# Kernel tuning notes

Measured on AMD Instinct MI355X. Metric: run time of the kernel, lower is better.

Reference implementation:

```python
import jax, jax.numpy as jnp
import numpy as np

NUM_CATS = 5
EPS = 1e-6


def setup_inputs() -> dict:
    key = jax.random.key(0)
    k1, k2, k3, k4 = jax.random.split(key, 4)
    B, C, H, W = 64, 3, 256, 256
    restored = jax.random.normal(k1, (B, C, H, W), dtype=jnp.float32)
    clean_patch_1 = jax.random.normal(k2, (B, C, H, W), dtype=jnp.float32)
    un = jax.random.uniform(k3, (B, C, H, W), dtype=jnp.float32)
    de_id = jax.random.randint(k4, (B,), 0, NUM_CATS)
    return {"restored": restored, "clean_patch_1": clean_patch_1,
            "de_id": de_id, "un": un}


def _loss(restored, clean, un, de_id):
    B, C, H, W = restored.shape
    E = C * H * W  # elements per sample
    dt = restored.dtype

    onehot = (de_id[:, None] == jnp.arange(NUM_CATS)[None, :])  # [B,5] bool
    m = onehot.astype(dt)                                        # [B,5]
    counts = onehot.sum(0)                                       # [5] int
    nonempty = counts > 0
    safe_counts = jnp.maximum(counts, 1).astype(dt)              # avoid 0-div

    # Per-category mean uncertainty map: un_map[c] = mean_{i: de_id[i]=c} un[i] + eps
    un_sum = jnp.einsum('bk,bchw->kchw', m, un)                  # [5,C,H,W]
    un_map = un_sum / safe_counts[:, None, None, None] + EPS     # [5,C,H,W]
    s = 1.0 / un_map                                             # [5,C,H,W]

    # Per-sample scaled L1 (s gathered by each sample's category)
    absdiff = jnp.abs(clean - restored)                          # [B,C,H,W]
    scaled_sum_per_sample = (absdiff * s[de_id]).sum(axis=(1, 2, 3))  # [B]
    abs_sum_per_sample = absdiff.sum(axis=(1, 2, 3))                  # [B]

    cat_scaled_sum = jnp.einsum('bk,b->k', m, scaled_sum_per_sample)  # [5]
    cat_abs_sum = jnp.einsum('bk,b->k', m, abs_sum_per_sample)        # [5]

    # NOTE: the original code never clears un_hq_list/un_lq_list between
    # categories, so the L1 at category c is the mean over ALL samples from
    # categories 0..c (each scaled by its OWN category's s). Replicate that
    # via cumulative sums/counts over the category axis.
    cum_scaled = jnp.cumsum(cat_scaled_sum)                      # [5]
    cum_elems = jnp.cumsum(counts).astype(dt) * E                # [5]
    cum_l1 = cum_scaled / jnp.maximum(cum_elems, 1.0)            # [5]

    old_loss = jnp.where(nonempty, cat_abs_sum / (safe_counts * E), 0.0)
    un_num = un_map.mean(axis=(1, 2, 3))                         # [5]
    bn = jnp.where(nonempty, 2.0 * jnp.log(un_num), 0.0)
    unc_l1 = jnp.where(nonempty, cum_l1, 0.0)

    cat_losses = unc_l1 + bn                                     # [5]
    num = nonempty.sum().astype(dt)
    total = cat_losses.sum() / num
    return total, cat_losses, old_loss, bn, unc_l1


def reference(restored, clean_patch_1, de_id, un):
    return _loss(restored, clean_patch_1, un, de_id)
```

## Files before the change

### kernel.cpp

```cpp
#include <hip/hip_runtime.h>
#include <math.h>

#define NCAT  5
#define BATCH 64
#define ELEMS 196608
#define EPSV  1e-6f

typedef float v4f __attribute__((ext_vector_type(4)));

#define WIN   1024
#define WIN4  (WIN / 4)
#define NCHK  4
#define NBLK1 (ELEMS / WIN)
#define CHUNK 16
#define GRP   4

#define NSLAB  12
#define SLABSZ (ELEMS / NSLAB)
#define NBLK2  (BATCH * NSLAB)

#define WS_S   0
#define WS_P1  (NCAT * ELEMS)
#define WS_P2  (WS_P1 + NCAT * NBLK1)

static __device__ __forceinline__ v4f vfma(float m, v4f a, v4f b) {
    v4f r;
    r.x = fmaf(m, a.x, b.x);
    r.y = fmaf(m, a.y, b.y);
    r.z = fmaf(m, a.z, b.z);
    r.w = fmaf(m, a.w, b.w);
    return r;
}

__global__ __launch_bounds__(256, 1) void pass1_kernel(
    const float* __restrict__ un,
    const int*   __restrict__ de_id,
    float*       __restrict__ s_buf,
    float*       __restrict__ p1)
{
    __shared__ int   sh_de[BATCH];
    __shared__ float sh_inv[NCAT];
    __shared__ v4f   sbuf[2][NCAT][WIN4];

    const int tid  = threadIdx.x;
    const int lane = tid & 63;
    const int wave = tid >> 6;

    if (tid < BATCH) {
        int k = de_id[tid];
        sh_de[tid] = k;
        #pragma unroll
        for (int j = 0; j < NCAT; ++j) {
            unsigned long long m = __ballot(k == j);
            if (tid == j) {
                int c = __popcll(m);
                sh_inv[j] = 1.0f / (float)(c > 0 ? c : 1);
            }
        }
    }
    __syncthreads();

    const size_t STR4 = ELEMS / 4;
    const v4f* up4 = (const v4f*)(un) + (size_t)blockIdx.x * WIN4 + lane;

    v4f acc[NCAT][NCHK];
    #pragma unroll
    for (int j = 0; j < NCAT; ++j)
        #pragma unroll
        for (int c = 0; c < NCHK; ++c) acc[j][c] = (v4f)0.f;

    v4f ub[2][GRP][NCHK];
    #pragma unroll
    for (int i = 0; i < GRP; ++i)
        #pragma unroll
        for (int c = 0; c < NCHK; ++c)
            ub[0][i][c] = up4[(size_t)(wave * CHUNK + i) * STR4 + c * 64];

    #pragma unroll
    for (int g = 0; g < CHUNK / GRP; ++g) {
        const int cur = g & 1;
        const int nxt = cur ^ 1;
        if (g < CHUNK / GRP - 1) {
            #pragma unroll
            for (int i = 0; i < GRP; ++i)
                #pragma unroll
                for (int c = 0; c < NCHK; ++c)
                    ub[nxt][i][c] =
                        up4[(size_t)(wave * CHUNK + (g + 1) * GRP + i) * STR4 + c * 64];
        }
        #pragma unroll
        for (int i = 0; i < GRP; ++i) {
            const int k = sh_de[wave * CHUNK + g * GRP + i];
            #pragma unroll
            for (int j = 0; j < NCAT; ++j) {
                float m = (k == j) ? 1.0f : 0.0f;
                #pragma unroll
                for (int c = 0; c < NCHK; ++c)
                    acc[j][c] = vfma(m, ub[cur][i][c], acc[j][c]);
            }
        }
    }

    if (wave >= 2) {
        #pragma unroll
        for (int j = 0; j < NCAT; ++j)
            #pragma unroll
            for (int c = 0; c < NCHK; ++c)
                sbuf[wave - 2][j][c * 64 + lane] = acc[j][c];
    }
    __syncthreads();
    if (wave < 2) {
        #pragma unroll
        for (int j = 0; j < NCAT; ++j)
            #pragma unroll
            for (int c = 0; c < NCHK; ++c)
                acc[j][c] += sbuf[wave][j][c * 64 + lane];
    }
    __syncthreads();
    if (wave == 1) {
        #pragma unroll
        for (int j = 0; j < NCAT; ++j)
            #pragma unroll
            for (int c = 0; c < NCHK; ++c)
                sbuf[0][j][c * 64 + lane] = acc[j][c];
    }
    __syncthreads();
    if (wave == 0) {
        float vals[NCAT];
        #pragma unroll
        for (int j = 0; j < NCAT; ++j) {
            float tot = 0.f;
            #pragma unroll
            for (int c = 0; c < NCHK; ++c) {
                v4f a = acc[j][c] + sbuf[0][j][c * 64 + lane];

                v4f um;
                um.x = fmaf(a.x, sh_inv[j], EPSV);
                um.y = fmaf(a.y, sh_inv[j], EPSV);
                um.z = fmaf(a.z, sh_inv[j], EPSV);
                um.w = fmaf(a.w, sh_inv[j], EPSV);
                v4f sv;
                sv.x = 1.0f / um.x;
                sv.y = 1.0f / um.y;
                sv.z = 1.0f / um.z;
                sv.w = 1.0f / um.w;
                ((v4f*)s_buf)[(size_t)j * STR4 + (size_t)blockIdx.x * WIN4
                              + c * 64 + lane] = sv;

                tot += (a.x + a.y) + (a.z + a.w);
            }
            vals[j] = tot;
        }

        #pragma unroll
        for (int i = 0; i < NCAT; ++i) {
            float v = vals[i];
            #pragma unroll
            for (int off = 32; off >= 1; off >>= 1)
                v += __shfl_down(v, off, 64);
            vals[i] = v;
        }
        if (lane == 0) {
            #pragma unroll
            for (int i = 0; i < NCAT; ++i)
                p1[i * NBLK1 + blockIdx.x] = vals[i];
        }
    }
}

__global__ __launch_bounds__(256) void pass2_kernel(
    const float* __restrict__ restored,
    const float* __restrict__ clean,
    const int*   __restrict__ de_id,
    const float* __restrict__ s_buf,
    float*       __restrict__ p2)
{
    __shared__ float sred[4][2];

    const int tid  = threadIdx.x;
    const int lane = tid & 63;
    const int wave = tid >> 6;

    const int b   = blockIdx.x / NSLAB;
    const int sl  = blockIdx.x % NSLAB;
    const int cat = de_id[b];

    const size_t base4 = (size_t)sl * (SLABSZ / 4) + (size_t)wave * (SLABSZ / 16)
                       + (size_t)lane;
    const v4f* cp = (const v4f*)(clean)    + (size_t)b   * (ELEMS / 4) + base4;
    const v4f* rp = (const v4f*)(restored) + (size_t)b   * (ELEMS / 4) + base4;
    const v4f* sp = (const v4f*)(s_buf)    + (size_t)cat * (ELEMS / 4) + base4;

    float ssum = 0.f, asum = 0.f;
    #pragma unroll 16
    for (int it = 0; it < SLABSZ / 16 / 64; ++it) {
        v4f c  = __builtin_nontemporal_load(cp + it * 64);
        v4f r  = __builtin_nontemporal_load(rp + it * 64);
        v4f sv = sp[it * 64];
        float a0 = fabsf(c.x - r.x);
        float a1 = fabsf(c.y - r.y);
        float a2 = fabsf(c.z - r.z);
        float a3 = fabsf(c.w - r.w);
        asum += (a0 + a1) + (a2 + a3);
        ssum = fmaf(a0, sv.x, ssum);
        ssum = fmaf(a1, sv.y, ssum);
        ssum = fmaf(a2, sv.z, ssum);
        ssum = fmaf(a3, sv.w, ssum);
    }

    #pragma unroll
    for (int off = 32; off >= 1; off >>= 1) {
        ssum += __shfl_down(ssum, off, 64);
        asum += __shfl_down(asum, off, 64);
    }
    if (lane == 0) { sred[wave][0] = ssum; sred[wave][1] = asum; }
    __syncthreads();
    if (tid == 0) {
        float s = sred[0][0] + sred[1][0] + sred[2][0] + sred[3][0];
        float a = sred[0][1] + sred[1][1] + sred[2][1] + sred[3][1];
        p2[blockIdx.x]         = s;
        p2[NBLK2 + blockIdx.x] = a;
    }
}

__global__ __launch_bounds__(1024) void epilogue_kernel(
    const int*   __restrict__ de_id,
    const float* __restrict__ p1,
    const float* __restrict__ p2,
    float*       __restrict__ out)
{
    __shared__ int   sh_cnt[NCAT];
    __shared__ int   sh_cat[BATCH];
    __shared__ float sh_acc[3 * NCAT];

    const int tid  = threadIdx.x;
    const int lane = tid & 63;
    const int wave = tid >> 6;

    if (tid < BATCH) {
        int k = de_id[tid];
        sh_cat[tid] = k;
        #pragma unroll
        for (int j = 0; j < NCAT; ++j) {
            unsigned long long m = __ballot(k == j);
            if (tid == j) sh_cnt[j] = __popcll(m);
        }
    }
    __syncthreads();

    float v = 0.f;
    if (wave < 5) {
        for (int it = 0; it < NBLK2 / 64; ++it) {
            int col = it * 64 + lane;
            v += (sh_cat[col / NSLAB] == wave) ? p2[col] : 0.f;
        }
    } else if (wave < 10) {
        const int j = wave - 5;
        for (int it = 0; it < NBLK2 / 64; ++it) {
            int col = it * 64 + lane;
            v += (sh_cat[col / NSLAB] == j) ? p2[NBLK2 + col] : 0.f;
        }
    } else if (wave < 15) {
        const int j = wave - 10;
        for (int it = 0; it < NBLK1 / 64; ++it)
            v += p1[j * NBLK1 + it * 64 + lane];
    }
    #pragma unroll
    for (int off = 32; off >= 1; off >>= 1)
        v += __shfl_down(v, off, 64);
    if (lane == 0 && wave < 15) sh_acc[wave] = v;
    __syncthreads();

    if (tid == 0) {
        const float Ef = (float)ELEMS;
        float cum_s = 0.f;
        long  cum_c = 0;
        float total = 0.f;
        int   num   = 0;

        float cat_losses[NCAT], old_loss[NCAT], bn[NCAT], unc_l1[NCAT];

        for (int j = 0; j < NCAT; ++j) {
            cum_s += sh_acc[j];
            cum_c += sh_cnt[j];
            float cum_elems = (float)cum_c * Ef;
            float cum_l1    = cum_s / fmaxf(cum_elems, 1.0f);

            bool  ne   = sh_cnt[j] > 0;
            float safe = (float)(ne ? sh_cnt[j] : 1);

            old_loss[j]  = ne ? sh_acc[NCAT + j] / (safe * Ef) : 0.f;
            float un_num = sh_acc[2 * NCAT + j] / (safe * Ef) + EPSV;
            bn[j]        = ne ? 2.0f * logf(un_num) : 0.f;
            unc_l1[j]    = ne ? cum_l1 : 0.f;
            cat_losses[j] = unc_l1[j] + bn[j];
            total += cat_losses[j];
            num   += ne ? 1 : 0;
        }
        total /= (float)num;

        out[0] = total;
        for (int j = 0; j < NCAT; ++j) {
            out[1 + j]  = cat_losses[j];
            out[6 + j]  = old_loss[j];
            out[11 + j] = bn[j];
            out[16 + j] = unc_l1[j];
        }
    }
}

extern "C" void kernel_launch(void* const* d_in, const int* in_sizes, int n_in,
                              void* d_out, int out_size, void* d_ws, size_t ws_size,
                              hipStream_t stream) {
    (void)in_sizes; (void)n_in; (void)out_size; (void)ws_size;
    const float* restored = (const float*)d_in[0];
    const float* clean    = (const float*)d_in[1];
    const int*   de_id    = (const int*)d_in[2];
    const float* un       = (const float*)d_in[3];
    float* out   = (float*)d_out;
    float* ws    = (float*)d_ws;
    float* s_buf = ws + WS_S;
    float* p1    = ws + WS_P1;
    float* p2    = ws + WS_P2;

    pass1_kernel<<<NBLK1, 256, 0, stream>>>(un, de_id, s_buf, p1);
    pass2_kernel<<<NBLK2, 256, 0, stream>>>(restored, clean, de_id, s_buf, p2);
    epilogue_kernel<<<1, 1024, 0, stream>>>(de_id, p1, p2, out);
}
```

Measured before the change: 168.8 us.

## Widen pass1 to 1024 threads and fold epilogue into pass2 via last-block atomic

Pass1 now runs 1024 threads per block, with each wave covering 64 float4 columns instead of four chunks. This cuts per-thread register use and raises the number of waves in flight for the un reduction. The separate epilogue launch is removed: the last pass2 block, detected with an atomic counter reset in pass1, performs the final category reduction. This saves one kernel launch and its serial gap, but adds a threadfence and an atomic to every pass2 block.

```diff
diff --git a/kernel.cpp b/kernel.cpp
--- a/kernel.cpp
+++ b/kernel.cpp
@@ -8,12 +8,11 @@
 
 typedef float v4f __attribute__((ext_vector_type(4)));
 
-#define WIN   1024
-#define WIN4  (WIN / 4)
-#define NCHK  4
-#define NBLK1 (ELEMS / WIN)
-#define CHUNK 16
-#define GRP   4
+#define WIN1   1024
+#define NBLK1  (ELEMS / WIN1)
+#define TPB1   1024
+#define CHUNK1 16
+#define GRP1   8
 
 #define NSLAB  12
 #define SLABSZ (ELEMS / NSLAB)
@@ -22,6 +21,7 @@
 #define WS_S   0
 #define WS_P1  (NCAT * ELEMS)
 #define WS_P2  (WS_P1 + NCAT * NBLK1)
+#define WS_CNT (WS_P2 + 2 * NBLK2)
 
 static __device__ __forceinline__ v4f vfma(float m, v4f a, v4f b) {
     v4f r;
@@ -32,19 +32,25 @@
     return r;
 }
 
-__global__ __launch_bounds__(256, 1) void pass1_kernel(
+__global__ __launch_bounds__(TPB1) void pass1_kernel(
     const float* __restrict__ un,
     const int*   __restrict__ de_id,
     float*       __restrict__ s_buf,
-    float*       __restrict__ p1)
+    float*       __restrict__ p1,
+    unsigned*    __restrict__ cnt)
 {
     __shared__ int   sh_de[BATCH];
     __shared__ float sh_inv[NCAT];
-    __shared__ v4f   sbuf[2][NCAT][WIN4];
+    __shared__ v4f   sbuf[2][4][NCAT][64];
+    __shared__ float sh_part[4][NCAT];
 
     const int tid  = threadIdx.x;
     const int lane = tid & 63;
     const int wave = tid >> 6;
+    const int ws   = wave & 3;
+    const int bc   = wave >> 2;
+
+    if (blockIdx.x == 0 && tid == 0) *cnt = 0u;
 
     if (tid < BATCH) {
         int k = de_id[tid];
@@ -61,111 +67,85 @@
     __syncthreads();
 
     const size_t STR4 = ELEMS / 4;
-    const v4f* up4 = (const v4f*)(un) + (size_t)blockIdx.x * WIN4 + lane;
-
-    v4f acc[NCAT][NCHK];
+    const size_t pos4 = (size_t)blockIdx.x * (WIN1 / 4) + ws * 64 + lane;
+    const v4f* up4 = (const v4f*)(un) + pos4;
+
+    v4f acc[NCAT];
     #pragma unroll
-    for (int j = 0; j < NCAT; ++j)
-        #pragma unroll
-        for (int c = 0; c < NCHK; ++c) acc[j][c] = (v4f)0.f;
-
-    v4f ub[2][GRP][NCHK];
+    for (int j = 0; j < NCAT; ++j) acc[j] = (v4f)0.f;
+
+    v4f ub[2][GRP1];
     #pragma unroll
-    for (int i = 0; i < GRP; ++i)
-        #pragma unroll
-        for (int c = 0; c < NCHK; ++c)
-            ub[0][i][c] = up4[(size_t)(wave * CHUNK + i) * STR4 + c * 64];
+    for (int i = 0; i < GRP1; ++i)
+        ub[0][i] = up4[(size_t)(bc * CHUNK1 + i) * STR4];
 
     #pragma unroll
-    for (int g = 0; g < CHUNK / GRP; ++g) {
+    for (int g = 0; g < CHUNK1 / GRP1; ++g) {
         const int cur = g & 1;
         const int nxt = cur ^ 1;
-        if (g < CHUNK / GRP - 1) {
-            #pragma unroll
-            for (int i = 0; i < GRP; ++i)
-                #pragma unroll
-                for (int c = 0; c < NCHK; ++c)
-                    ub[nxt][i][c] =
-                        up4[(size_t)(wave * CHUNK + (g + 1) * GRP + i) * STR4 + c * 64];
-        }
-        #pragma unroll
-        for (int i = 0; i < GRP; ++i) {
-            const int k = sh_de[wave * CHUNK + g * GRP + i];
+        if (g < CHUNK1 / GRP1 - 1) {
+            #pragma unroll
+            for (int i = 0; i < GRP1; ++i)
+                ub[nxt][i] = up4[(size_t)(bc * CHUNK1 + (g + 1) * GRP1 + i) * STR4];
+        }
+        #pragma unroll
+        for (int i = 0; i < GRP1; ++i) {
+            const int k = sh_de[bc * CHUNK1 + g * GRP1 + i];
             #pragma unroll
             for (int j = 0; j < NCAT; ++j) {
                 float m = (k == j) ? 1.0f : 0.0f;
-                #pragma unroll
-                for (int c = 0; c < NCHK; ++c)
-                    acc[j][c] = vfma(m, ub[cur][i][c], acc[j][c]);
+                acc[j] = vfma(m, ub[cur][i], acc[j]);
             }
         }
     }
 
-    if (wave >= 2) {
-        #pragma unroll
-        for (int j = 0; j < NCAT; ++j)
-            #pragma unroll
-            for (int c = 0; c < NCHK; ++c)
-                sbuf[wave - 2][j][c * 64 + lane] = acc[j][c];
-    }
-    __syncthreads();
-    if (wave < 2) {
-        #pragma unroll
-        for (int j = 0; j < NCAT; ++j)
-            #pragma unroll
-            for (int c = 0; c < NCHK; ++c)
-                acc[j][c] += sbuf[wave][j][c * 64 + lane];
-    }
-    __syncthreads();
-    if (wave == 1) {
-        #pragma unroll
-        for (int j = 0; j < NCAT; ++j)
-            #pragma unroll
-            for (int c = 0; c < NCHK; ++c)
-                sbuf[0][j][c * 64 + lane] = acc[j][c];
-    }
-    __syncthreads();
-    if (wave == 0) {
+    if (bc >= 2) {
+        #pragma unroll
+        for (int j = 0; j < NCAT; ++j) sbuf[bc - 2][ws][j][lane] = acc[j];
+    }
+    __syncthreads();
+    if (bc < 2) {
+        #pragma unroll
+        for (int j = 0; j < NCAT; ++j) acc[j] += sbuf[bc][ws][j][lane];
+    }
+    __syncthreads();
+    if (bc == 1) {
+        #pragma unroll
+        for (int j = 0; j < NCAT; ++j) sbuf[0][ws][j][lane] = acc[j];
+    }
+    __syncthreads();
+    if (bc == 0) {
         float vals[NCAT];
         #pragma unroll
         for (int j = 0; j < NCAT; ++j) {
-            float tot = 0.f;
-            #pragma unroll
-            for (int c = 0; c < NCHK; ++c) {
-                v4f a = acc[j][c] + sbuf[0][j][c * 64 + lane];
-
-                v4f um;
-                um.x = fmaf(a.x, sh_inv[j], EPSV);
-                um.y = fmaf(a.y, sh_inv[j], EPSV);
-                um.z = fmaf(a.z, sh_inv[j], EPSV);
-                um.w = fmaf(a.w, sh_inv[j], EPSV);
-                v4f sv;
-                sv.x = 1.0f / um.x;
-                sv.y = 1.0f / um.y;
-                sv.z = 1.0f / um.z;
-                sv.w = 1.0f / um.w;
-                ((v4f*)s_buf)[(size_t)j * STR4 + (size_t)blockIdx.x * WIN4
-                              + c * 64 + lane] = sv;
-
-                tot += (a.x + a.y) + (a.z + a.w);
-            }
-            vals[j] = tot;
-        }
-
-        #pragma unroll
-        for (int i = 0; i < NCAT; ++i) {
-            float v = vals[i];
+            v4f a = acc[j] + sbuf[0][ws][j][lane];
+
+            v4f um, sv;
+            um.x = fmaf(a.x, sh_inv[j], EPSV);
+            um.y = fmaf(a.y, sh_inv[j], EPSV);
+            um.z = fmaf(a.z, sh_inv[j], EPSV);
+            um.w = fmaf(a.w, sh_inv[j], EPSV);
+            sv.x = 1.0f / um.x;
+            sv.y = 1.0f / um.y;
+            sv.z = 1.0f / um.z;
+            sv.w = 1.0f / um.w;
+            ((v4f*)s_buf)[(size_t)j * STR4 + pos4] = sv;
+
+            vals[j] = (a.x + a.y) + (a.z + a.w);
+        }
+        #pragma unroll
+        for (int j = 0; j < NCAT; ++j) {
+            float v = vals[j];
             #pragma unroll
             for (int off = 32; off >= 1; off >>= 1)
                 v += __shfl_down(v, off, 64);
-            vals[i] = v;
-        }
-        if (lane == 0) {
-            #pragma unroll
-            for (int i = 0; i < NCAT; ++i)
-                p1[i * NBLK1 + blockIdx.x] = vals[i];
-        }
-    }
+            if (lane == 0) sh_part[ws][j] = v;
+        }
+    }
+    __syncthreads();
+    if (tid < NCAT)
+        p1[tid * NBLK1 + blockIdx.x] =
+            sh_part[0][tid] + sh_part[1][tid] + sh_part[2][tid] + sh_part[3][tid];
 }
 
 __global__ __launch_bounds__(256) void pass2_kernel(
@@ -173,9 +153,16 @@
     const float* __restrict__ clean,
     const int*   __restrict__ de_id,
     const float* __restrict__ s_buf,
-    float*       __restrict__ p2)
+    float*       __restrict__ p1,
+    float*       __restrict__ p2,
+    unsigned*    __restrict__ cnt,
+    float*       __restrict__ out)
 {
     __shared__ float sred[4][2];
+    __shared__ int   sh_last;
+    __shared__ int   sh_cat[BATCH];
+    __shared__ int   sh_cnt[NCAT];
+    __shared__ float sh_acc[3 * NCAT];
 
     const int tid  = threadIdx.x;
     const int lane = tid & 63;
@@ -220,22 +207,12 @@
         float a = sred[0][1] + sred[1][1] + sred[2][1] + sred[3][1];
         p2[blockIdx.x]         = s;
         p2[NBLK2 + blockIdx.x] = a;
-    }
-}
-
-__global__ __launch_bounds__(1024) void epilogue_kernel(
-    const int*   __restrict__ de_id,
-    const float* __restrict__ p1,
-    const float* __restrict__ p2,
-    float*       __restrict__ out)
-{
-    __shared__ int   sh_cnt[NCAT];
-    __shared__ int   sh_cat[BATCH];
-    __shared__ float sh_acc[3 * NCAT];
-
-    const int tid  = threadIdx.x;
-    const int lane = tid & 63;
-    const int wave = tid >> 6;
+        __threadfence();
+        unsigned old = atomicAdd(cnt, 1u);
+        sh_last = (old == NBLK2 - 1) ? 1 : 0;
+    }
+    __syncthreads();
+    if (!sh_last) return;
 
     if (tid < BATCH) {
         int k = de_id[tid];
@@ -248,27 +225,39 @@
     }
     __syncthreads();
 
-    float v = 0.f;
-    if (wave < 5) {
+    if (wave < 2) {
+        const float* src = (wave == 0) ? p2 : p2 + NBLK2;
+        float accv[NCAT] = {0.f, 0.f, 0.f, 0.f, 0.f};
         for (int it = 0; it < NBLK2 / 64; ++it) {
-            int col = it * 64 + lane;
-            v += (sh_cat[col / NSLAB] == wave) ? p2[col] : 0.f;
-        }
-    } else if (wave < 10) {
-        const int j = wave - 5;
-        for (int it = 0; it < NBLK2 / 64; ++it) {
-            int col = it * 64 + lane;
-            v += (sh_cat[col / NSLAB] == j) ? p2[NBLK2 + col] : 0.f;
-        }
-    } else if (wave < 15) {
-        const int j = wave - 10;
+            int   col = it * 64 + lane;
+            float v   = src[col];
+            int   c   = sh_cat[col / NSLAB];
+            #pragma unroll
+            for (int j = 0; j < NCAT; ++j) accv[j] += (c == j) ? v : 0.f;
+        }
+        #pragma unroll
+        for (int j = 0; j < NCAT; ++j) {
+            float v = accv[j];
+            #pragma unroll
+            for (int off = 32; off >= 1; off >>= 1)
+                v += __shfl_down(v, off, 64);
+            if (lane == 0) sh_acc[wave * NCAT + j] = v;
+        }
+    } else if (wave == 2) {
+        float accv[NCAT] = {0.f, 0.f, 0.f, 0.f, 0.f};
         for (int it = 0; it < NBLK1 / 64; ++it)
-            v += p1[j * NBLK1 + it * 64 + lane];
-    }
-    #pragma unroll
-    for (int off = 32; off >= 1; off >>= 1)
-        v += __shfl_down(v, off, 64);
-    if (lane == 0 && wave < 15) sh_acc[wave] = v;
+            #pragma unroll
+            for (int j = 0; j < NCAT; ++j)
+                accv[j] += p1[j * NBLK1 + it * 64 + lane];
+        #pragma unroll
+        for (int j = 0; j < NCAT; ++j) {
+            float v = accv[j];
+            #pragma unroll
+            for (int off = 32; off >= 1; off >>= 1)
+                v += __shfl_down(v, off, 64);
+            if (lane == 0) sh_acc[2 * NCAT + j] = v;
+        }
+    }
     __syncthreads();
 
     if (tid == 0) {
@@ -319,11 +308,12 @@
     const float* un       = (const float*)d_in[3];
     float* out   = (float*)d_out;
     float* ws    = (float*)d_ws;
-    float* s_buf = ws + WS_S;
-    float* p1    = ws + WS_P1;
-    float* p2    = ws + WS_P2;
-
-    pass1_kernel<<<NBLK1, 256, 0, stream>>>(un, de_id, s_buf, p1);
-    pass2_kernel<<<NBLK2, 256, 0, stream>>>(restored, clean, de_id, s_buf, p2);
-    epilogue_kernel<<<1, 1024, 0, stream>>>(de_id, p1, p2, out);
+    float*    s_buf = ws + WS_S;
+    float*    p1    = ws + WS_P1;
+    float*    p2    = ws + WS_P2;
+    unsigned* cnt   = (unsigned*)(ws + WS_CNT);
+
+    pass1_kernel<<<NBLK1, TPB1, 0, stream>>>(un, de_id, s_buf, p1, cnt);
+    pass2_kernel<<<NBLK2, 256, 0, stream>>>(restored, clean, de_id, s_buf,
+                                            p1, p2, cnt, out);
 }
```

New measurement: 201.2 us. +19.2%, slower.
